# Kernel tuning notes

Hardware: AMD Instinct MI355X
Metric: run time of the kernel (lower is better)

Reference implementation:

```python
import jax, jax.numpy as jnp
import numpy as np

B = 256      # events
N_SV = 64    # secondary vertices per event
N_TRK = 512  # tracks per event
N_PFC = 512  # PF candidates per event
K = 8        # kNN neighbors
H = 32       # hidden dim


def _lin_init(key, fan_in, fan_out):
    k1, k2 = jax.random.split(key)
    lim = 1.0 / np.sqrt(fan_in)
    W = jax.random.uniform(k1, (fan_in, fan_out), minval=-lim, maxval=lim, dtype=jnp.float32)
    b = jax.random.uniform(k2, (fan_out,), minval=-lim, maxval=lim, dtype=jnp.float32)
    return W, b


def setup_inputs() -> dict:
    key = jax.random.key(0)
    ks = jax.random.split(key, 16)
    inp = {
        'x_sv': jax.random.normal(ks[0], (B * N_SV, 14), dtype=jnp.float32),
        'x_trk': jax.random.normal(ks[1], (B * N_TRK, 30), dtype=jnp.float32),
        'x_pfc': jax.random.normal(ks[2], (B * N_PFC, 10), dtype=jnp.float32),
        'batch_sv': jnp.repeat(jnp.arange(B, dtype=jnp.int64), N_SV),
        'batch_trk': jnp.repeat(jnp.arange(B, dtype=jnp.int64), N_TRK),
        'batch_pfc': jnp.repeat(jnp.arange(B, dtype=jnp.int64), N_PFC),
    }
    inp['sv_W1'], inp['sv_b1'] = _lin_init(ks[3], 14, H)
    inp['sv_W2'], inp['sv_b2'] = _lin_init(ks[4], H, H)
    inp['trk_W1'], inp['trk_b1'] = _lin_init(ks[5], 30, H)
    inp['trk_W2'], inp['trk_b2'] = _lin_init(ks[6], H, H)
    inp['pfc_W1'], inp['pfc_b1'] = _lin_init(ks[7], 10, H)
    inp['pfc_W2'], inp['pfc_b2'] = _lin_init(ks[8], H, H)
    inp['conv_W'], inp['conv_b'] = _lin_init(ks[9], 2 * H, H)  # the single shared self.conv
    inp['out_W1'], inp['out_b1'] = _lin_init(ks[10], H, H)
    inp['out_W2'], inp['out_b2'] = _lin_init(ks[11], H, 1)
    return inp


def _encode(x, W1, b1, W2, b2):
    h = jax.nn.elu(x @ W1 + b1)
    return jax.nn.elu(h @ W2 + b2)


def _edge_conv(x_src, x_dst, W, b):
    # x_src [B,Ns,H] source set, x_dst [B,Nd,H] destination/query set.
    # kNN: for each dst node, K nearest src nodes (per event) by Euclidean dist.
    d2 = (jnp.sum(x_dst * x_dst, -1)[:, :, None]
          - 2.0 * jnp.einsum('bnd,bmd->bnm', x_dst, x_src)
          + jnp.sum(x_src * x_src, -1)[:, None, :])  # [B,Nd,Ns]
    _, idx = jax.lax.top_k(-d2, K)                     # [B,Nd,K]
    x_j = jax.vmap(lambda s, i: s[i])(x_src, idx)      # [B,Nd,K,H]
    x_i = jnp.broadcast_to(x_dst[:, :, None, :], x_j.shape)
    e = jnp.concatenate([x_i, x_j - x_i], axis=-1)     # [B,Nd,K,2H]
    m = jax.nn.elu(e @ W + b)                          # edge MLP
    return jnp.max(m, axis=2)                          # max aggregation [B,Nd,H]


def reference(x_sv, x_trk, x_pfc, batch_sv, batch_trk, batch_pfc,
              sv_W1, sv_b1, sv_W2, sv_b2,
              trk_W1, trk_b1, trk_W2, trk_b2,
              pfc_W1, pfc_b1, pfc_W2, pfc_b2,
              conv_W, conv_b, out_W1, out_b1, out_W2, out_b2):
    sv = _encode(x_sv, sv_W1, sv_b1, sv_W2, sv_b2).reshape(B, N_SV, H)
    trk = _encode(x_trk, trk_W1, trk_b1, trk_W2, trk_b2).reshape(B, N_TRK, H)
    pfc = _encode(x_pfc, pfc_W1, pfc_b1, pfc_W2, pfc_b2).reshape(B, N_PFC, H)

    feats1 = _edge_conv(sv, trk, conv_W, conv_b)     # sv -> trk
    feats2 = _edge_conv(pfc, trk, conv_W, conv_b)    # pfc -> trk
    feats3 = _edge_conv(feats1, feats2, conv_W, conv_b)  # feats1 -> feats2 (both trk-sized)

    # avg_pool_x(batch_trk, feats3, batch_trk): per-event mean
    f = feats3.reshape(B * N_TRK, H)
    s = jax.ops.segment_sum(f, batch_trk, num_segments=B)
    cnt = jax.ops.segment_sum(jnp.ones((B * N_TRK,), f.dtype), batch_trk, num_segments=B)
    pooled = s / cnt[:, None]

    out = jax.nn.sigmoid(jax.nn.elu(pooled @ out_W1 + out_b1) @ out_W2 + out_b2)  # [B,1]
    return out, jnp.arange(B, dtype=jnp.int64)
```

## Files before the change

kernel.cpp:

```cpp
#include <hip/hip_runtime.h>
#include <math.h>

#define NB 256
#define KNN 8

typedef __attribute__((ext_vector_type(8))) short short8;
typedef __attribute__((ext_vector_type(4))) float f32x4;

__device__ __forceinline__ float elu_f(float x) {
    return x > 0.f ? x : __expf(x) - 1.f;
}

__device__ __forceinline__ unsigned bf16rn(float x) {
    unsigned u = __float_as_uint(x);
    return (u + 0x7FFFu + ((u >> 16) & 1u)) >> 16;
}

__device__ __forceinline__ void bfsplit(float x, short& h, short& l) {
    unsigned hu = bf16rn(x);
    h = (short)hu;
    l = (short)bf16rn(x - __uint_as_float(hu << 16));
}

__device__ __forceinline__ void cex(unsigned& a, unsigned& b) {
    unsigned lo = min(a, b), hi = max(a, b);
    a = lo; b = hi;
}

__device__ __forceinline__ void sort8(unsigned* s) {
    cex(s[0], s[1]); cex(s[2], s[3]); cex(s[4], s[5]); cex(s[6], s[7]);
    cex(s[0], s[2]); cex(s[1], s[3]); cex(s[4], s[6]); cex(s[5], s[7]);
    cex(s[1], s[2]); cex(s[5], s[6]);
    cex(s[0], s[4]); cex(s[1], s[5]); cex(s[2], s[6]); cex(s[3], s[7]);
    cex(s[2], s[4]); cex(s[3], s[5]);
    cex(s[1], s[2]); cex(s[3], s[4]); cex(s[5], s[6]);
}

__device__ __forceinline__ void merge8(unsigned* v, const unsigned* s) {
#pragma unroll
    for (int i = 0; i < 8; i++) v[i] = min(v[i], s[7 - i]);
    cex(v[0], v[4]); cex(v[1], v[5]); cex(v[2], v[6]); cex(v[3], v[7]);
    cex(v[0], v[2]); cex(v[1], v[3]); cex(v[4], v[6]); cex(v[5], v[7]);
    cex(v[0], v[1]); cex(v[2], v[3]); cex(v[4], v[5]); cex(v[6], v[7]);
}

template<int FIN, int MODE>
__device__ void encode_mfma_body(const float* __restrict__ x,
    const float* __restrict__ W1, const float* __restrict__ b1,
    const float* __restrict__ W2, const float* __restrict__ b2,
    const float* __restrict__ conv_W, const float* __restrict__ conv_b,
    float* __restrict__ enc, float* __restrict__ e1, float* __restrict__ e2,
    unsigned short* __restrict__ hiP, unsigned short* __restrict__ loP,
    float* __restrict__ nrmP,
    int blk, float* __restrict__ sx)
{
    int tid = threadIdx.x;
    int lane = tid & 63, wv = tid >> 6;
    int c = lane & 15, kg = lane >> 4;
    size_t node0 = (size_t)blk * 256;

    {
        const float* xb = x + node0 * FIN;
        for (int i = tid; i < 8192; i += 256) {
            int n = i >> 5, f = i & 31;
            sx[i] = (f < FIN) ? xb[n * FIN + f] : 0.f;
        }
    }
    __syncthreads();

    int rb = wv * 64;

#pragma unroll
    for (int ph = 0; ph < 3; ph++) {
        short8 Bh0, Bl0, Bh1, Bl1;
#pragma unroll
        for (int e = 0; e < 8; e++) {
            int kk = kg * 8 + e;
            float w0, w1;
            if (ph == 0) {
                w0 = (kk < FIN) ? W1[kk * 32 + c] : 0.f;
                w1 = (kk < FIN) ? W1[kk * 32 + 16 + c] : 0.f;
            } else if (ph == 1) {
                w0 = W2[kk * 32 + c];
                w1 = W2[kk * 32 + 16 + c];
            } else {
                w0 = conv_W[1024 + kk * 32 + c];
                w1 = conv_W[1024 + kk * 32 + 16 + c];
                if (MODE == 1) {
                    w0 = conv_W[kk * 32 + c] - w0;
                    w1 = conv_W[kk * 32 + 16 + c] - w1;
                }
            }
            short h, l;
            bfsplit(w0, h, l); Bh0[e] = h; Bl0[e] = l;
            bfsplit(w1, h, l); Bh1[e] = h; Bl1[e] = l;
        }
        float bias0, bias1;
        if (ph == 0)      { bias0 = b1[c]; bias1 = b1[16 + c]; }
        else if (ph == 1) { bias0 = b2[c]; bias1 = b2[16 + c]; }
        else              { bias0 = (MODE == 1) ? conv_b[c] : 0.f;
                            bias1 = (MODE == 1) ? conv_b[16 + c] : 0.f; }

#pragma unroll
        for (int t = 0; t < 4; t++) {
            int tb = rb + t * 16;
            int arow = tb + c;
            const float* ap = sx + arow * 32 + kg * 8;
            float4 a0 = *(const float4*)(ap);
            float4 a1 = *(const float4*)(ap + 4);
            float av[8] = {a0.x, a0.y, a0.z, a0.w, a1.x, a1.y, a1.z, a1.w};
            short8 Ah, Al;
#pragma unroll
            for (int e = 0; e < 8; e++) {
                short h, l;
                bfsplit(av[e], h, l);
                Ah[e] = h; Al[e] = l;
            }

            if (MODE == 0 && ph == 2) {
                float nr = 0.f;
#pragma unroll
                for (int e = 0; e < 8; e++) nr = fmaf(av[e], av[e], nr);
                nr += __shfl_xor(nr, 16);
                nr += __shfl_xor(nr, 32);
                if (kg == 0) nrmP[node0 + arow] = nr;
                *(short8*)(hiP + (node0 + arow) * 32 + kg * 8) = Ah;
                *(short8*)(loP + (node0 + arow) * 32 + kg * 8) = Al;
            }

            f32x4 acc0 = {bias0, bias0, bias0, bias0};
            f32x4 acc1 = {bias1, bias1, bias1, bias1};
            acc0 = __builtin_amdgcn_mfma_f32_16x16x32_bf16(Al, Bh0, acc0, 0, 0, 0);
            acc0 = __builtin_amdgcn_mfma_f32_16x16x32_bf16(Ah, Bl0, acc0, 0, 0, 0);
            acc0 = __builtin_amdgcn_mfma_f32_16x16x32_bf16(Ah, Bh0, acc0, 0, 0, 0);
            acc1 = __builtin_amdgcn_mfma_f32_16x16x32_bf16(Al, Bh1, acc1, 0, 0, 0);
            acc1 = __builtin_amdgcn_mfma_f32_16x16x32_bf16(Ah, Bl1, acc1, 0, 0, 0);
            acc1 = __builtin_amdgcn_mfma_f32_16x16x32_bf16(Ah, Bh1, acc1, 0, 0, 0);

            int drow = tb + kg * 4;
            if (ph < 2) {
#pragma unroll
                for (int r = 0; r < 4; r++) {
                    float v0 = elu_f(acc0[r]);
                    float v1 = elu_f(acc1[r]);
                    sx[(drow + r) * 32 + c] = v0;
                    sx[(drow + r) * 32 + 16 + c] = v1;
                    if (MODE == 1 && ph == 1) {
                        size_t off = (node0 + drow + r) * 32 + c;
                        enc[off] = v0;
                        enc[off + 16] = v1;
                    }
                }
            } else {
#pragma unroll
                for (int r = 0; r < 4; r++) {
                    size_t off = (node0 + drow + r) * 32 + c;
                    e1[off] = acc0[r];
                    e1[off + 16] = acc1[r];
                    if (MODE == 1) {
                        e2[off] = acc0[r];
                        e2[off + 16] = acc1[r];
                    }
                }
            }
        }
    }
}

__global__ __launch_bounds__(256) void encode_all_kernel(
    const float* __restrict__ x_sv, const float* __restrict__ x_trk, const float* __restrict__ x_pfc,
    const float* __restrict__ sv_W1, const float* __restrict__ sv_b1,
    const float* __restrict__ sv_W2, const float* __restrict__ sv_b2,
    const float* __restrict__ trk_W1, const float* __restrict__ trk_b1,
    const float* __restrict__ trk_W2, const float* __restrict__ trk_b2,
    const float* __restrict__ pfc_W1, const float* __restrict__ pfc_b1,
    const float* __restrict__ pfc_W2, const float* __restrict__ pfc_b2,
    const float* __restrict__ conv_W, const float* __restrict__ conv_b,
    float* __restrict__ trk_enc,
    float* __restrict__ Y1, float* __restrict__ Y2,
    float* __restrict__ f1, float* __restrict__ f2,
    unsigned short* __restrict__ svHi, unsigned short* __restrict__ svLo, float* __restrict__ nrm_sv,
    unsigned short* __restrict__ pfcHi, unsigned short* __restrict__ pfcLo, float* __restrict__ nrm_pfc)
{
    __shared__ float sx[8192];
    int bid = blockIdx.x;
    if (bid < 64)
        encode_mfma_body<14, 0>(x_sv, sv_W1, sv_b1, sv_W2, sv_b2, conv_W, conv_b,
                                nullptr, Y1, nullptr, svHi, svLo, nrm_sv, bid, sx);
    else if (bid < 576)
        encode_mfma_body<30, 1>(x_trk, trk_W1, trk_b1, trk_W2, trk_b2, conv_W, conv_b,
                                trk_enc, f1, f2, nullptr, nullptr, nullptr, bid - 64, sx);
    else
        encode_mfma_body<10, 0>(x_pfc, pfc_W1, pfc_b1, pfc_W2, pfc_b2, conv_W, conv_b,
                                nullptr, Y2, nullptr, pfcHi, pfcLo, nrm_pfc, bid - 576, sx);
}

__device__ __forceinline__ void knn_build_B(const float* __restrict__ dstF,
                                            int dstbase, int c, int kg,
                                            short8& Bh, short8& Bl, float& nd)
{
    const float* brow = dstF + (size_t)(dstbase + c) * 32 + kg * 8;
    float4 b0 = *(const float4*)(brow);
    float4 b1 = *(const float4*)(brow + 4);
    float bx[8] = {b0.x, b0.y, b0.z, b0.w, b1.x, b1.y, b1.z, b1.w};
    nd = 0.f;
#pragma unroll
    for (int i = 0; i < 8; i++) {
        float xv = bx[i];
        nd = fmaf(xv, xv, nd);
        short h, l;
        bfsplit(xv, h, l);
        Bh[i] = h; Bl[i] = l;
    }
    nd += __shfl_xor(nd, 16);
    nd += __shfl_xor(nd, 32);
}

template<int NT>
__device__ __forceinline__ void knn_scan(
    const unsigned short* __restrict__ srcHi, const unsigned short* __restrict__ srcLo,
    const float* __restrict__ snrm,
    short8 Bh, short8 Bl, float nd, int c, int kg,
    unsigned* key)
{
    for (int t = 0; t < NT; t += 2) {
        unsigned cand[8];
#pragma unroll
        for (int u = 0; u < 2; u++) {
            int tt = t + u;
            size_t arow = ((size_t)(tt * 16 + c)) * 32 + (size_t)kg * 8;
            short8 Ah = *(const short8*)(srcHi + arow);
            short8 Al = *(const short8*)(srcLo + arow);
            f32x4 acc = {0.f, 0.f, 0.f, 0.f};
            acc = __builtin_amdgcn_mfma_f32_16x16x32_bf16(Al, Bl, acc, 0, 0, 0);
            acc = __builtin_amdgcn_mfma_f32_16x16x32_bf16(Al, Bh, acc, 0, 0, 0);
            acc = __builtin_amdgcn_mfma_f32_16x16x32_bf16(Ah, Bl, acc, 0, 0, 0);
            acc = __builtin_amdgcn_mfma_f32_16x16x32_bf16(Ah, Bh, acc, 0, 0, 0);
            float4 sn = *(const float4*)(snrm + tt * 16 + kg * 4);
            int sb = tt * 16 + kg * 4;
            cand[u*4+0] = (__float_as_uint(fmaf(-2.f, acc[0], sn.x + nd)) & 0xFFFFFE00u) | (unsigned)(sb + 0);
            cand[u*4+1] = (__float_as_uint(fmaf(-2.f, acc[1], sn.y + nd)) & 0xFFFFFE00u) | (unsigned)(sb + 1);
            cand[u*4+2] = (__float_as_uint(fmaf(-2.f, acc[2], sn.z + nd)) & 0xFFFFFE00u) | (unsigned)(sb + 2);
            cand[u*4+3] = (__float_as_uint(fmaf(-2.f, acc[3], sn.w + nd)) & 0xFFFFFE00u) | (unsigned)(sb + 3);
        }
        sort8(cand);
        merge8(key, cand);
    }
}

__device__ __forceinline__ void knn_finalize(unsigned* key, int lane,
                                             unsigned short* __restrict__ idx_out,
                                             int dstbase)
{
    unsigned oth[8];
#pragma unroll
    for (int k = 0; k < 8; k++) oth[k] = __shfl_xor(key[k], 16);
    merge8(key, oth);
#pragma unroll
    for (int k = 0; k < 8; k++) oth[k] = __shfl_xor(key[k], 32);
    merge8(key, oth);
    if (lane < 16) {
        uint4 o;
        o.x = (key[0] & 511u) | ((key[1] & 511u) << 16);
        o.y = (key[2] & 511u) | ((key[3] & 511u) << 16);
        o.z = (key[4] & 511u) | ((key[5] & 511u) << 16);
        o.w = (key[6] & 511u) | ((key[7] & 511u) << 16);
        *(uint4*)(idx_out + (size_t)(dstbase + lane) * 8) = o;
    }
}

__global__ __launch_bounds__(256) void knn12_kernel(
    const unsigned short* __restrict__ svHi, const unsigned short* __restrict__ svLo,
    const float* __restrict__ nrm_sv,
    const unsigned short* __restrict__ pfcHi, const unsigned short* __restrict__ pfcLo,
    const float* __restrict__ nrm_pfc,
    const float* __restrict__ trk_enc,
    unsigned short* __restrict__ idx1, unsigned short* __restrict__ idx2)
{
    int bid = blockIdx.x;
    int e = bid & 255, j = bid >> 8;
    int lane = threadIdx.x & 63, wave = threadIdx.x >> 6;
    int c = lane & 15, kg = lane >> 4;
    int dstbase = j * 64 + wave * 16;

    short8 Bh, Bl;
    float nd;
    knn_build_B(trk_enc + (size_t)e * 512 * 32, dstbase, c, kg, Bh, Bl, nd);

    unsigned key[8];
#pragma unroll
    for (int k = 0; k < 8; k++) key[k] = 0xFFFFFFFFu;
    knn_scan<32>(pfcHi + (size_t)e * 512 * 32, pfcLo + (size_t)e * 512 * 32,
                 nrm_pfc + e * 512, Bh, Bl, nd, c, kg, key);
    knn_finalize(key, lane, idx2 + (size_t)e * 512 * 8, dstbase);

#pragma unroll
    for (int k = 0; k < 8; k++) key[k] = 0xFFFFFFFFu;
    knn_scan<4>(svHi + (size_t)e * 64 * 32, svLo + (size_t)e * 64 * 32,
                nrm_sv + e * 64, Bh, Bl, nd, c, kg, key);
    knn_finalize(key, lane, idx1 + (size_t)e * 512 * 8, dstbase);
}

__global__ __launch_bounds__(256) void knn3_kernel(
    const unsigned short* __restrict__ f1Hi, const unsigned short* __restrict__ f1Lo,
    const float* __restrict__ nrm_f1,
    const float* __restrict__ f2,
    unsigned short* __restrict__ idx3)
{
    int bid = blockIdx.x;
    int e = bid & 255, j = bid >> 8;
    int lane = threadIdx.x & 63, wave = threadIdx.x >> 6;
    int c = lane & 15, kg = lane >> 4;
    int dstbase = j * 64 + wave * 16;

    short8 Bh, Bl;
    float nd;
    knn_build_B(f2 + (size_t)e * 512 * 32, dstbase, c, kg, Bh, Bl, nd);

    unsigned key[8];
#pragma unroll
    for (int k = 0; k < 8; k++) key[k] = 0xFFFFFFFFu;
    knn_scan<32>(f1Hi + (size_t)e * 512 * 32, f1Lo + (size_t)e * 512 * 32,
                 nrm_f1 + e * 512, Bh, Bl, nd, c, kg, key);
    knn_finalize(key, lane, idx3 + (size_t)e * 512 * 8, dstbase);
}

__device__ __forceinline__ void maxgather(const float* __restrict__ Ybase,
                                          const int* rows, float4* m)
{
    const float4* Yb = (const float4*)Ybase;
    const float4* r0 = Yb + (size_t)rows[0] * 8;
#pragma unroll
    for (int q = 0; q < 8; q++) m[q] = r0[q];
#pragma unroll
    for (int k = 1; k < 8; k++) {
        const float4* rr = Yb + (size_t)rows[k] * 8;
#pragma unroll
        for (int q = 0; q < 8; q++) {
            float4 v = rr[q];
            m[q].x = fmaxf(m[q].x, v.x); m[q].y = fmaxf(m[q].y, v.y);
            m[q].z = fmaxf(m[q].z, v.z); m[q].w = fmaxf(m[q].w, v.w);
        }
    }
}

__device__ __forceinline__ void decode_rows(const unsigned short* __restrict__ ip,
                                            size_t t, int* rows)
{
    uint4 u = *(const uint4*)(ip + t * 8);
    rows[0] = (int)(u.x & 0xffff); rows[1] = (int)(u.x >> 16);
    rows[2] = (int)(u.y & 0xffff); rows[3] = (int)(u.y >> 16);
    rows[4] = (int)(u.z & 0xffff); rows[5] = (int)(u.z >> 16);
    rows[6] = (int)(u.w & 0xffff); rows[7] = (int)(u.w >> 16);
}

__global__ __launch_bounds__(256) void g12_kernel(
    const float* __restrict__ Y1, const unsigned short* __restrict__ idx1, float* __restrict__ f1,
    const float* __restrict__ Y2, const unsigned short* __restrict__ idx2, float* __restrict__ f2,
    unsigned short* __restrict__ f1Hi, unsigned short* __restrict__ f1Lo,
    float* __restrict__ nrm_f1)
{
    int bid = blockIdx.x;
    int tid = threadIdx.x;
    int rows[8];
    float* fp;
    const float* Yb;
    int t;
    int isf1 = (bid < 512);
    if (isf1) {
        t = bid * 256 + tid;
        decode_rows(idx1, (size_t)t, rows);
        Yb = Y1 + (size_t)(t >> 9) * 64 * 32;
        fp = f1 + (size_t)t * 32;
    } else {
        t = (bid - 512) * 256 + tid;
        decode_rows(idx2, (size_t)t, rows);
        Yb = Y2 + (size_t)(t >> 9) * 512 * 32;
        fp = f2 + (size_t)t * 32;
    }
    float4 m[8];
    maxgather(Yb, rows, m);
    float4* op = (float4*)fp;
    float4 r[8];
#pragma unroll
    for (int q = 0; q < 8; q++) {
        float4 bv = op[q];
        r[q].x = elu_f(bv.x + m[q].x); r[q].y = elu_f(bv.y + m[q].y);
        r[q].z = elu_f(bv.z + m[q].z); r[q].w = elu_f(bv.w + m[q].w);
        op[q] = r[q];
    }
    if (isf1) {
        unsigned hw[16], lw[16];
        float nr = 0.f;
#pragma unroll
        for (int q = 0; q < 8; q++) {
            float4 v = r[q];
            nr = fmaf(v.x, v.x, nr); nr = fmaf(v.y, v.y, nr);
            nr = fmaf(v.z, v.z, nr); nr = fmaf(v.w, v.w, nr);
            unsigned h0 = bf16rn(v.x), h1 = bf16rn(v.y), h2 = bf16rn(v.z), h3 = bf16rn(v.w);
            unsigned l0 = bf16rn(v.x - __uint_as_float(h0 << 16));
            unsigned l1 = bf16rn(v.y - __uint_as_float(h1 << 16));
            unsigned l2 = bf16rn(v.z - __uint_as_float(h2 << 16));
            unsigned l3 = bf16rn(v.w - __uint_as_float(h3 << 16));
            hw[2*q]   = h0 | (h1 << 16); hw[2*q+1] = h2 | (h3 << 16);
            lw[2*q]   = l0 | (l1 << 16); lw[2*q+1] = l2 | (l3 << 16);
        }
        nrm_f1[t] = nr;
        uint4* hp = (uint4*)(f1Hi + (size_t)t * 32);
        uint4* lp = (uint4*)(f1Lo + (size_t)t * 32);
#pragma unroll
        for (int q = 0; q < 4; q++) {
            hp[q] = make_uint4(hw[4*q], hw[4*q+1], hw[4*q+2], hw[4*q+3]);
            lp[q] = make_uint4(lw[4*q], lw[4*q+1], lw[4*q+2], lw[4*q+3]);
        }
    }
}

__global__ __launch_bounds__(256) void yb3_kernel(
    const float* __restrict__ f1, const float* __restrict__ f2,
    const float* __restrict__ conv_W, const float* __restrict__ conv_b,
    float* __restrict__ Y3, float* __restrict__ B3)
{
    int bid = blockIdx.x;
    int mode = (bid >= 512);
    const float* X = mode ? f2 : f1;
    float* O = mode ? B3 : Y3;
    size_t node0 = (size_t)(mode ? bid - 512 : bid) * 256;
    int tid = threadIdx.x, lane = tid & 63, wv = tid >> 6;
    int c = lane & 15, kg = lane >> 4;

    short8 Bh0, Bl0, Bh1, Bl1;
#pragma unroll
    for (int e = 0; e < 8; e++) {
        int kk = kg * 8 + e;
        float w0 = conv_W[1024 + kk * 32 + c];
        float w1 = conv_W[1024 + kk * 32 + 16 + c];
        if (mode) {
            w0 = conv_W[kk * 32 + c] - w0;
            w1 = conv_W[kk * 32 + 16 + c] - w1;
        }
        short h, l;
        bfsplit(w0, h, l); Bh0[e] = h; Bl0[e] = l;
        bfsplit(w1, h, l); Bh1[e] = h; Bl1[e] = l;
    }
    float bias0 = mode ? conv_b[c] : 0.f;
    float bias1 = mode ? conv_b[16 + c] : 0.f;

    int rb = wv * 64;
#pragma unroll
    for (int t = 0; t < 4; t++) {
        int tb = rb + t * 16;
        int arow = tb + c;
        const float* ap = X + (node0 + arow) * 32 + kg * 8;
        float4 a0 = *(const float4*)(ap);
        float4 a1 = *(const float4*)(ap + 4);
        float av[8] = {a0.x, a0.y, a0.z, a0.w, a1.x, a1.y, a1.z, a1.w};
        short8 Ah, Al;
#pragma unroll
        for (int e = 0; e < 8; e++) {
            short h, l;
            bfsplit(av[e], h, l);
            Ah[e] = h; Al[e] = l;
        }
        f32x4 acc0 = {bias0, bias0, bias0, bias0};
        f32x4 acc1 = {bias1, bias1, bias1, bias1};
        acc0 = __builtin_amdgcn_mfma_f32_16x16x32_bf16(Al, Bh0, acc0, 0, 0, 0);
        acc0 = __builtin_amdgcn_mfma_f32_16x16x32_bf16(Ah, Bl0, acc0, 0, 0, 0);
        acc0 = __builtin_amdgcn_mfma_f32_16x16x32_bf16(Ah, Bh0, acc0, 0, 0, 0);
        acc1 = __builtin_amdgcn_mfma_f32_16x16x32_bf16(Al, Bh1, acc1, 0, 0, 0);
        acc1 = __builtin_amdgcn_mfma_f32_16x16x32_bf16(Ah, Bl1, acc1, 0, 0, 0);
        acc1 = __builtin_amdgcn_mfma_f32_16x16x32_bf16(Ah, Bh1, acc1, 0, 0, 0);

        int drow = tb + kg * 4;
#pragma unroll
        for (int r = 0; r < 4; r++) {
            size_t off = (node0 + drow + r) * 32 + c;
            O[off] = acc0[r];
            O[off + 16] = acc1[r];
        }
    }
}

__global__ __launch_bounds__(256) void g3_kernel(
    const float* __restrict__ Y3, const float* __restrict__ B3,
    const unsigned short* __restrict__ idx3,
    float* __restrict__ pool)
{
    __shared__ float sp[4][32];
    int bid = blockIdx.x;
    int tid = threadIdx.x, lane = tid & 63, wave = tid >> 6;
    int t = bid * 256 + tid;
    int e = t >> 9;
    int rows[8];
    decode_rows(idx3, (size_t)t, rows);
    float4 m[8];
    maxgather(Y3 + (size_t)e * 512 * 32, rows, m);
    const float4* bp = (const float4*)(B3 + (size_t)t * 32);
    float4 r[8];
#pragma unroll
    for (int q = 0; q < 8; q++) {
        float4 bv = bp[q];
        r[q].x = elu_f(bv.x + m[q].x); r[q].y = elu_f(bv.y + m[q].y);
        r[q].z = elu_f(bv.z + m[q].z); r[q].w = elu_f(bv.w + m[q].w);
    }
    for (int off = 1; off < 64; off <<= 1) {
#pragma unroll
        for (int q = 0; q < 8; q++) {
            r[q].x += __shfl_xor(r[q].x, off);
            r[q].y += __shfl_xor(r[q].y, off);
            r[q].z += __shfl_xor(r[q].z, off);
            r[q].w += __shfl_xor(r[q].w, off);
        }
    }
    if (lane == 0) {
#pragma unroll
        for (int q = 0; q < 8; q++) {
            sp[wave][q*4+0] = r[q].x; sp[wave][q*4+1] = r[q].y;
            sp[wave][q*4+2] = r[q].z; sp[wave][q*4+3] = r[q].w;
        }
    }
    __syncthreads();
    if (tid < 32)
        pool[(size_t)bid * 32 + tid] = sp[0][tid] + sp[1][tid] + sp[2][tid] + sp[3][tid];
}

__global__ __launch_bounds__(64) void final_kernel(
    const float* __restrict__ pool,
    const float* __restrict__ W1, const float* __restrict__ b1,
    const float* __restrict__ W2, const float* __restrict__ b2,
    float* __restrict__ outp)
{
    int b = blockIdx.x;
    int lane = threadIdx.x, c = lane & 31;
    __shared__ float sp[32];
    __shared__ float sh1[32];
    if (lane < 32)
        sp[c] = (pool[(size_t)(2*b) * 32 + c] + pool[(size_t)(2*b+1) * 32 + c]) * (1.0f / 512.0f);
    __syncthreads();
    if (lane < 32) {
        float h = b1[c];
#pragma unroll
        for (int d = 0; d < 32; d++) h = fmaf(sp[d], W1[d * 32 + c], h);
        sh1[c] = elu_f(h);
    }
    __syncthreads();
    if (lane == 0) {
        float o = b2[0];
#pragma unroll
        for (int d = 0; d < 32; d++) o = fmaf(sh1[d], W2[d], o);
        o = 1.f / (1.f + __expf(-o));
        outp[b] = o;
        outp[NB + b] = (float)b;
    }
}

extern "C" void kernel_launch(void* const* d_in, const int* in_sizes, int n_in,
                              void* d_out, int out_size, void* d_ws, size_t ws_size,
                              hipStream_t stream) {
    const float* x_sv  = (const float*)d_in[0];
    const float* x_trk = (const float*)d_in[1];
    const float* x_pfc = (const float*)d_in[2];
    const float* sv_W1  = (const float*)d_in[6];
    const float* sv_b1  = (const float*)d_in[7];
    const float* sv_W2  = (const float*)d_in[8];
    const float* sv_b2  = (const float*)d_in[9];
    const float* trk_W1 = (const float*)d_in[10];
    const float* trk_b1 = (const float*)d_in[11];
    const float* trk_W2 = (const float*)d_in[12];
    const float* trk_b2 = (const float*)d_in[13];
    const float* pfc_W1 = (const float*)d_in[14];
    const float* pfc_b1 = (const float*)d_in[15];
    const float* pfc_W2 = (const float*)d_in[16];
    const float* pfc_b2 = (const float*)d_in[17];
    const float* conv_W = (const float*)d_in[18];
    const float* conv_b = (const float*)d_in[19];
    const float* out_W1 = (const float*)d_in[20];
    const float* out_b1 = (const float*)d_in[21];
    const float* out_W2 = (const float*)d_in[22];
    const float* out_b2 = (const float*)d_in[23];

    float* ws = (float*)d_ws;
    const size_t SV_E  = (size_t)NB * 64 * 32;
    const size_t TRK_E = (size_t)NB * 512 * 32;
    float* f1      = ws;
    float* f2      = f1 + TRK_E;
    float* trk_enc = f2 + TRK_E;
    float* Y1      = trk_enc + TRK_E;
    float* Y2      = Y1 + SV_E;
    unsigned short* svHi  = (unsigned short*)(Y2 + TRK_E);
    unsigned short* svLo  = svHi + SV_E;
    unsigned short* pfcHi = svLo + SV_E;
    unsigned short* pfcLo = pfcHi + TRK_E;
    unsigned short* f1Hi  = pfcLo + TRK_E;
    unsigned short* f1Lo  = f1Hi + TRK_E;
    float* nrm_sv  = (float*)(f1Lo + TRK_E);
    float* nrm_pfc = nrm_sv + (size_t)NB * 64;
    float* nrm_f1  = nrm_pfc + (size_t)NB * 512;
    unsigned short* idx1 = (unsigned short*)(nrm_f1 + (size_t)NB * 512);
    unsigned short* idx2 = idx1 + (size_t)NB * 512 * 8;
    unsigned short* idx3 = idx2 + (size_t)NB * 512 * 8;
    float* Y3   = trk_enc;
    float* B3   = (float*)pfcHi;
    float* pool = (float*)svHi;

    encode_all_kernel<<<1088, 256, 0, stream>>>(
        x_sv, x_trk, x_pfc,
        sv_W1, sv_b1, sv_W2, sv_b2,
        trk_W1, trk_b1, trk_W2, trk_b2,
        pfc_W1, pfc_b1, pfc_W2, pfc_b2,
        conv_W, conv_b,
        trk_enc, Y1, Y2, f1, f2,
        svHi, svLo, nrm_sv, pfcHi, pfcLo, nrm_pfc);

    knn12_kernel<<<2048, 256, 0, stream>>>(svHi, svLo, nrm_sv,
                                           pfcHi, pfcLo, nrm_pfc,
                                           trk_enc, idx1, idx2);
    g12_kernel<<<1024, 256, 0, stream>>>(Y1, idx1, f1, Y2, idx2, f2,
                                         f1Hi, f1Lo, nrm_f1);

    yb3_kernel<<<1024, 256, 0, stream>>>(f1, f2, conv_W, conv_b, Y3, B3);
    knn3_kernel<<<2048, 256, 0, stream>>>(f1Hi, f1Lo, nrm_f1, f2, idx3);
    g3_kernel<<<512, 256, 0, stream>>>(Y3, B3, idx3, pool);

    final_kernel<<<NB, 64, 0, stream>>>(pool, out_W1, out_b1, out_W2, out_b2, (float*)d_out);
}
```

Baseline: 316.3 us.

## Fuse kNN gather-max aggregation into kNN kernels, drop index buffers

The separate gather/max kernels (g12, g3) are folded into the kNN kernels. After the lanes merge their top-8 keys, each lane gathers its 8-float slice of the neighbor rows, applies the max, bias and ELU, and writes features, the bf16 hi/lo splits and norms directly. Pooling becomes a per-block partial sum that final_kernel adds across 8 blocks. This removes two launches, the idx1/2/3 round trips and the duplicate f2 write in the encoder. In exchange, gather latency moves into the kNN kernels and adds register pressure there.

After: 303.9 us. -3.9%, faster.

```diff
diff --git a/kernel.cpp b/kernel.cpp
--- a/kernel.cpp
+++ b/kernel.cpp
@@ -49,7 +49,7 @@
     const float* __restrict__ W1, const float* __restrict__ b1,
     const float* __restrict__ W2, const float* __restrict__ b2,
     const float* __restrict__ conv_W, const float* __restrict__ conv_b,
-    float* __restrict__ enc, float* __restrict__ e1, float* __restrict__ e2,
+    float* __restrict__ enc, float* __restrict__ e1,
     unsigned short* __restrict__ hiP, unsigned short* __restrict__ loP,
     float* __restrict__ nrmP,
     int blk, float* __restrict__ sx)
@@ -157,10 +157,6 @@
                     size_t off = (node0 + drow + r) * 32 + c;
                     e1[off] = acc0[r];
                     e1[off + 16] = acc1[r];
-                    if (MODE == 1) {
-                        e2[off] = acc0[r];
-                        e2[off + 16] = acc1[r];
-                    }
                 }
             }
         }
@@ -178,7 +174,7 @@
     const float* __restrict__ conv_W, const float* __restrict__ conv_b,
     float* __restrict__ trk_enc,
     float* __restrict__ Y1, float* __restrict__ Y2,
-    float* __restrict__ f1, float* __restrict__ f2,
+    float* __restrict__ f1,
     unsigned short* __restrict__ svHi, unsigned short* __restrict__ svLo, float* __restrict__ nrm_sv,
     unsigned short* __restrict__ pfcHi, unsigned short* __restrict__ pfcLo, float* __restrict__ nrm_pfc)
 {
@@ -186,13 +182,13 @@
     int bid = blockIdx.x;
     if (bid < 64)
         encode_mfma_body<14, 0>(x_sv, sv_W1, sv_b1, sv_W2, sv_b2, conv_W, conv_b,
-                                nullptr, Y1, nullptr, svHi, svLo, nrm_sv, bid, sx);
+                                nullptr, Y1, svHi, svLo, nrm_sv, bid, sx);
     else if (bid < 576)
         encode_mfma_body<30, 1>(x_trk, trk_W1, trk_b1, trk_W2, trk_b2, conv_W, conv_b,
-                                trk_enc, f1, f2, nullptr, nullptr, nullptr, bid - 64, sx);
+                                trk_enc, f1, nullptr, nullptr, nullptr, bid - 64, sx);
     else
         encode_mfma_body<10, 0>(x_pfc, pfc_W1, pfc_b1, pfc_W2, pfc_b2, conv_W, conv_b,
-                                nullptr, Y2, nullptr, pfcHi, pfcLo, nrm_pfc, bid - 576, sx);
+                                nullptr, Y2, pfcHi, pfcLo, nrm_pfc, bid - 576, sx);
 }
 
 __device__ __forceinline__ void knn_build_B(const float* __restrict__ dstF,
@@ -248,9 +244,7 @@
     }
 }
 
-__device__ __forceinline__ void knn_finalize(unsigned* key, int lane,
-                                             unsigned short* __restrict__ idx_out,
-                                             int dstbase)
+__device__ __forceinline__ void knn_merge_lanes(unsigned* key)
 {
     unsigned oth[8];
 #pragma unroll
@@ -259,13 +253,25 @@
 #pragma unroll
     for (int k = 0; k < 8; k++) oth[k] = __shfl_xor(key[k], 32);
     merge8(key, oth);
-    if (lane < 16) {
-        uint4 o;
-        o.x = (key[0] & 511u) | ((key[1] & 511u) << 16);
-        o.y = (key[2] & 511u) | ((key[3] & 511u) << 16);
-        o.z = (key[4] & 511u) | ((key[5] & 511u) << 16);
-        o.w = (key[6] & 511u) | ((key[7] & 511u) << 16);
-        *(uint4*)(idx_out + (size_t)(dstbase + lane) * 8) = o;
+}
+
+__device__ __forceinline__ void gather_max8(const float* __restrict__ Yb,
+                                            const unsigned* key, int kg, float* m)
+{
+    const float* r0 = Yb + (size_t)(key[0] & 511u) * 32 + kg * 8;
+    float4 a = *(const float4*)(r0);
+    float4 b = *(const float4*)(r0 + 4);
+    m[0] = a.x; m[1] = a.y; m[2] = a.z; m[3] = a.w;
+    m[4] = b.x; m[5] = b.y; m[6] = b.z; m[7] = b.w;
+#pragma unroll
+    for (int k = 1; k < 8; k++) {
+        const float* rr = Yb + (size_t)(key[k] & 511u) * 32 + kg * 8;
+        float4 va = *(const float4*)(rr);
+        float4 vb = *(const float4*)(rr + 4);
+        m[0] = fmaxf(m[0], va.x); m[1] = fmaxf(m[1], va.y);
+        m[2] = fmaxf(m[2], va.z); m[3] = fmaxf(m[3], va.w);
+        m[4] = fmaxf(m[4], vb.x); m[5] = fmaxf(m[5], vb.y);
+        m[6] = fmaxf(m[6], vb.z); m[7] = fmaxf(m[7], vb.w);
     }
 }
 
@@ -275,43 +281,91 @@
     const unsigned short* __restrict__ pfcHi, const unsigned short* __restrict__ pfcLo,
     const float* __restrict__ nrm_pfc,
     const float* __restrict__ trk_enc,
-    unsigned short* __restrict__ idx1, unsigned short* __restrict__ idx2)
+    const float* __restrict__ Y1, const float* __restrict__ Y2,
+    float* __restrict__ f1, float* __restrict__ f2,
+    unsigned short* __restrict__ f1Hi, unsigned short* __restrict__ f1Lo,
+    float* __restrict__ nrm_f1)
 {
     int bid = blockIdx.x;
     int e = bid & 255, j = bid >> 8;
     int lane = threadIdx.x & 63, wave = threadIdx.x >> 6;
     int c = lane & 15, kg = lane >> 4;
     int dstbase = j * 64 + wave * 16;
+    size_t trow = (size_t)e * 512 + dstbase + c;
 
     short8 Bh, Bl;
     float nd;
     knn_build_B(trk_enc + (size_t)e * 512 * 32, dstbase, c, kg, Bh, Bl, nd);
 
-    unsigned key[8];
-#pragma unroll
-    for (int k = 0; k < 8; k++) key[k] = 0xFFFFFFFFu;
+    unsigned key2[8];
+#pragma unroll
+    for (int k = 0; k < 8; k++) key2[k] = 0xFFFFFFFFu;
     knn_scan<32>(pfcHi + (size_t)e * 512 * 32, pfcLo + (size_t)e * 512 * 32,
-                 nrm_pfc + e * 512, Bh, Bl, nd, c, kg, key);
-    knn_finalize(key, lane, idx2 + (size_t)e * 512 * 8, dstbase);
-
-#pragma unroll
-    for (int k = 0; k < 8; k++) key[k] = 0xFFFFFFFFu;
+                 nrm_pfc + e * 512, Bh, Bl, nd, c, kg, key2);
+    knn_merge_lanes(key2);
+
+    unsigned key1[8];
+#pragma unroll
+    for (int k = 0; k < 8; k++) key1[k] = 0xFFFFFFFFu;
     knn_scan<4>(svHi + (size_t)e * 64 * 32, svLo + (size_t)e * 64 * 32,
-                nrm_sv + e * 64, Bh, Bl, nd, c, kg, key);
-    knn_finalize(key, lane, idx1 + (size_t)e * 512 * 8, dstbase);
+                nrm_sv + e * 64, Bh, Bl, nd, c, kg, key1);
+    knn_merge_lanes(key1);
+
+    const float* bp = f1 + trow * 32 + kg * 8;
+    float4 bb0 = *(const float4*)(bp);
+    float4 bb1 = *(const float4*)(bp + 4);
+    float base[8] = {bb0.x, bb0.y, bb0.z, bb0.w, bb1.x, bb1.y, bb1.z, bb1.w};
+
+    float m[8];
+    gather_max8(Y2 + (size_t)e * 512 * 32, key2, kg, m);
+    {
+        float4 o0, o1;
+        o0.x = elu_f(base[0] + m[0]); o0.y = elu_f(base[1] + m[1]);
+        o0.z = elu_f(base[2] + m[2]); o0.w = elu_f(base[3] + m[3]);
+        o1.x = elu_f(base[4] + m[4]); o1.y = elu_f(base[5] + m[5]);
+        o1.z = elu_f(base[6] + m[6]); o1.w = elu_f(base[7] + m[7]);
+        float4* op = (float4*)(f2 + trow * 32 + kg * 8);
+        op[0] = o0; op[1] = o1;
+    }
+    gather_max8(Y1 + (size_t)e * 64 * 32, key1, kg, m);
+    {
+        float v[8];
+        float nr = 0.f;
+        short8 Hh, Hl;
+#pragma unroll
+        for (int i = 0; i < 8; i++) {
+            v[i] = elu_f(base[i] + m[i]);
+            nr = fmaf(v[i], v[i], nr);
+            short h, l;
+            bfsplit(v[i], h, l);
+            Hh[i] = h; Hl[i] = l;
+        }
+        nr += __shfl_xor(nr, 16);
+        nr += __shfl_xor(nr, 32);
+        if (kg == 0) nrm_f1[trow] = nr;
+        float4* op = (float4*)(f1 + trow * 32 + kg * 8);
+        op[0] = (float4){v[0], v[1], v[2], v[3]};
+        op[1] = (float4){v[4], v[5], v[6], v[7]};
+        *(short8*)(f1Hi + trow * 32 + kg * 8) = Hh;
+        *(short8*)(f1Lo + trow * 32 + kg * 8) = Hl;
+    }
 }
 
 __global__ __launch_bounds__(256) void knn3_kernel(
     const unsigned short* __restrict__ f1Hi, const unsigned short* __restrict__ f1Lo,
     const float* __restrict__ nrm_f1,
     const float* __restrict__ f2,
-    unsigned short* __restrict__ idx3)
-{
+    const float* __restrict__ Y3, const float* __restrict__ B3,
+    float* __restrict__ pool)
+{
+    __shared__ float sp[4][32];
     int bid = blockIdx.x;
     int e = bid & 255, j = bid >> 8;
-    int lane = threadIdx.x & 63, wave = threadIdx.x >> 6;
+    int tid = threadIdx.x;
+    int lane = tid & 63, wave = tid >> 6;
     int c = lane & 15, kg = lane >> 4;
     int dstbase = j * 64 + wave * 16;
+    size_t trow = (size_t)e * 512 + dstbase + c;
 
     short8 Bh, Bl;
     float nd;
@@ -322,98 +376,33 @@
     for (int k = 0; k < 8; k++) key[k] = 0xFFFFFFFFu;
     knn_scan<32>(f1Hi + (size_t)e * 512 * 32, f1Lo + (size_t)e * 512 * 32,
                  nrm_f1 + e * 512, Bh, Bl, nd, c, kg, key);
-    knn_finalize(key, lane, idx3 + (size_t)e * 512 * 8, dstbase);
-}
-
-__device__ __forceinline__ void maxgather(const float* __restrict__ Ybase,
-                                          const int* rows, float4* m)
-{
-    const float4* Yb = (const float4*)Ybase;
-    const float4* r0 = Yb + (size_t)rows[0] * 8;
-#pragma unroll
-    for (int q = 0; q < 8; q++) m[q] = r0[q];
-#pragma unroll
-    for (int k = 1; k < 8; k++) {
-        const float4* rr = Yb + (size_t)rows[k] * 8;
-#pragma unroll
-        for (int q = 0; q < 8; q++) {
-            float4 v = rr[q];
-            m[q].x = fmaxf(m[q].x, v.x); m[q].y = fmaxf(m[q].y, v.y);
-            m[q].z = fmaxf(m[q].z, v.z); m[q].w = fmaxf(m[q].w, v.w);
-        }
-    }
-}
-
-__device__ __forceinline__ void decode_rows(const unsigned short* __restrict__ ip,
-                                            size_t t, int* rows)
-{
-    uint4 u = *(const uint4*)(ip + t * 8);
-    rows[0] = (int)(u.x & 0xffff); rows[1] = (int)(u.x >> 16);
-    rows[2] = (int)(u.y & 0xffff); rows[3] = (int)(u.y >> 16);
-    rows[4] = (int)(u.z & 0xffff); rows[5] = (int)(u.z >> 16);
-    rows[6] = (int)(u.w & 0xffff); rows[7] = (int)(u.w >> 16);
-}
-
-__global__ __launch_bounds__(256) void g12_kernel(
-    const float* __restrict__ Y1, const unsigned short* __restrict__ idx1, float* __restrict__ f1,
-    const float* __restrict__ Y2, const unsigned short* __restrict__ idx2, float* __restrict__ f2,
-    unsigned short* __restrict__ f1Hi, unsigned short* __restrict__ f1Lo,
-    float* __restrict__ nrm_f1)
-{
-    int bid = blockIdx.x;
-    int tid = threadIdx.x;
-    int rows[8];
-    float* fp;
-    const float* Yb;
-    int t;
-    int isf1 = (bid < 512);
-    if (isf1) {
-        t = bid * 256 + tid;
-        decode_rows(idx1, (size_t)t, rows);
-        Yb = Y1 + (size_t)(t >> 9) * 64 * 32;
-        fp = f1 + (size_t)t * 32;
-    } else {
-        t = (bid - 512) * 256 + tid;
-        decode_rows(idx2, (size_t)t, rows);
-        Yb = Y2 + (size_t)(t >> 9) * 512 * 32;
-        fp = f2 + (size_t)t * 32;
-    }
-    float4 m[8];
-    maxgather(Yb, rows, m);
-    float4* op = (float4*)fp;
-    float4 r[8];
-#pragma unroll
-    for (int q = 0; q < 8; q++) {
-        float4 bv = op[q];
-        r[q].x = elu_f(bv.x + m[q].x); r[q].y = elu_f(bv.y + m[q].y);
-        r[q].z = elu_f(bv.z + m[q].z); r[q].w = elu_f(bv.w + m[q].w);
-        op[q] = r[q];
-    }
-    if (isf1) {
-        unsigned hw[16], lw[16];
-        float nr = 0.f;
-#pragma unroll
-        for (int q = 0; q < 8; q++) {
-            float4 v = r[q];
-            nr = fmaf(v.x, v.x, nr); nr = fmaf(v.y, v.y, nr);
-            nr = fmaf(v.z, v.z, nr); nr = fmaf(v.w, v.w, nr);
-            unsigned h0 = bf16rn(v.x), h1 = bf16rn(v.y), h2 = bf16rn(v.z), h3 = bf16rn(v.w);
-            unsigned l0 = bf16rn(v.x - __uint_as_float(h0 << 16));
-            unsigned l1 = bf16rn(v.y - __uint_as_float(h1 << 16));
-            unsigned l2 = bf16rn(v.z - __uint_as_float(h2 << 16));
-            unsigned l3 = bf16rn(v.w - __uint_as_float(h3 << 16));
-            hw[2*q]   = h0 | (h1 << 16); hw[2*q+1] = h2 | (h3 << 16);
-            lw[2*q]   = l0 | (l1 << 16); lw[2*q+1] = l2 | (l3 << 16);
-        }
-        nrm_f1[t] = nr;
-        uint4* hp = (uint4*)(f1Hi + (size_t)t * 32);
-        uint4* lp = (uint4*)(f1Lo + (size_t)t * 32);
-#pragma unroll
-        for (int q = 0; q < 4; q++) {
-            hp[q] = make_uint4(hw[4*q], hw[4*q+1], hw[4*q+2], hw[4*q+3]);
-            lp[q] = make_uint4(lw[4*q], lw[4*q+1], lw[4*q+2], lw[4*q+3]);
-        }
-    }
+    knn_merge_lanes(key);
+
+    float m[8];
+    gather_max8(Y3 + (size_t)e * 512 * 32, key, kg, m);
+
+    const float* bp = B3 + trow * 32 + kg * 8;
+    float4 bb0 = *(const float4*)(bp);
+    float4 bb1 = *(const float4*)(bp + 4);
+    float base[8] = {bb0.x, bb0.y, bb0.z, bb0.w, bb1.x, bb1.y, bb1.z, bb1.w};
+
+    float r[8];
+#pragma unroll
+    for (int i = 0; i < 8; i++) r[i] = elu_f(base[i] + m[i]);
+
+#pragma unroll
+    for (int off = 1; off < 16; off <<= 1) {
+#pragma unroll
+        for (int i = 0; i < 8; i++) r[i] += __shfl_xor(r[i], off);
+    }
+    if (c == 0) {
+#pragma unroll
+        for (int i = 0; i < 8; i++) sp[wave][kg * 8 + i] = r[i];
+    }
+    __syncthreads();
+    if (tid < 32)
+        pool[((size_t)e * 8 + j) * 32 + tid] =
+            sp[0][tid] + sp[1][tid] + sp[2][tid] + sp[3][tid];
 }
 
 __global__ __launch_bounds__(256) void yb3_kernel(
@@ -481,49 +470,6 @@
     }
 }
 
-__global__ __launch_bounds__(256) void g3_kernel(
-    const float* __restrict__ Y3, const float* __restrict__ B3,
-    const unsigned short* __restrict__ idx3,
-    float* __restrict__ pool)
-{
-    __shared__ float sp[4][32];
-    int bid = blockIdx.x;
-    int tid = threadIdx.x, lane = tid & 63, wave = tid >> 6;
-    int t = bid * 256 + tid;
-    int e = t >> 9;
-    int rows[8];
-    decode_rows(idx3, (size_t)t, rows);
-    float4 m[8];
-    maxgather(Y3 + (size_t)e * 512 * 32, rows, m);
-    const float4* bp = (const float4*)(B3 + (size_t)t * 32);
-    float4 r[8];
-#pragma unroll
-    for (int q = 0; q < 8; q++) {
-        float4 bv = bp[q];
-        r[q].x = elu_f(bv.x + m[q].x); r[q].y = elu_f(bv.y + m[q].y);
-        r[q].z = elu_f(bv.z + m[q].z); r[q].w = elu_f(bv.w + m[q].w);
-    }
-    for (int off = 1; off < 64; off <<= 1) {
-#pragma unroll
-        for (int q = 0; q < 8; q++) {
-            r[q].x += __shfl_xor(r[q].x, off);
-            r[q].y += __shfl_xor(r[q].y, off);
-            r[q].z += __shfl_xor(r[q].z, off);
-            r[q].w += __shfl_xor(r[q].w, off);
-        }
-    }
-    if (lane == 0) {
-#pragma unroll
-        for (int q = 0; q < 8; q++) {
-            sp[wave][q*4+0] = r[q].x; sp[wave][q*4+1] = r[q].y;
-            sp[wave][q*4+2] = r[q].z; sp[wave][q*4+3] = r[q].w;
-        }
-    }
-    __syncthreads();
-    if (tid < 32)
-        pool[(size_t)bid * 32 + tid] = sp[0][tid] + sp[1][tid] + sp[2][tid] + sp[3][tid];
-}
-
 __global__ __launch_bounds__(64) void final_kernel(
     const float* __restrict__ pool,
     const float* __restrict__ W1, const float* __restrict__ b1,
@@ -534,8 +480,13 @@
     int lane = threadIdx.x, c = lane & 31;
     __shared__ float sp[32];
     __shared__ float sh1[32];
-    if (lane < 32)
-        sp[c] = (pool[(size_t)(2*b) * 32 + c] + pool[(size_t)(2*b+1) * 32 + c]) * (1.0f / 512.0f);
+    if (lane < 32) {
+        float s = 0.f;
+#pragma unroll
+        for (int jj = 0; jj < 8; jj++)
+            s += pool[((size_t)b * 8 + jj) * 32 + c];
+        sp[c] = s * (1.0f / 512.0f);
+    }
     __syncthreads();
     if (lane < 32) {
         float h = b1[c];
@@ -596,9 +547,6 @@
     float* nrm_sv  = (float*)(f1Lo + TRK_E);
     float* nrm_pfc = nrm_sv + (size_t)NB * 64;
     float* nrm_f1  = nrm_pfc + (size_t)NB * 512;
-    unsigned short* idx1 = (unsigned short*)(nrm_f1 + (size_t)NB * 512);
-    unsigned short* idx2 = idx1 + (size_t)NB * 512 * 8;
-    unsigned short* idx3 = idx2 + (size_t)NB * 512 * 8;
     float* Y3   = trk_enc;
     float* B3   = (float*)pfcHi;
     float* pool = (float*)svHi;
@@ -609,18 +557,16 @@
         trk_W1, trk_b1, trk_W2, trk_b2,
         pfc_W1, pfc_b1, pfc_W2, pfc_b2,
         conv_W, conv_b,
-        trk_enc, Y1, Y2, f1, f2,
+        trk_enc, Y1, Y2, f1,
         svHi, svLo, nrm_sv, pfcHi, pfcLo, nrm_pfc);
 
     knn12_kernel<<<2048, 256, 0, stream>>>(svHi, svLo, nrm_sv,
                                            pfcHi, pfcLo, nrm_pfc,
-                                           trk_enc, idx1, idx2);
-    g12_kernel<<<1024, 256, 0, stream>>>(Y1, idx1, f1, Y2, idx2, f2,
-                                         f1Hi, f1Lo, nrm_f1);
+                                           trk_enc, Y1, Y2,
+                                           f1, f2, f1Hi, f1Lo, nrm_f1);
 
     yb3_kernel<<<1024, 256, 0, stream>>>(f1, f2, conv_W, conv_b, Y3, B3);
-    knn3_kernel<<<2048, 256, 0, stream>>>(f1Hi, f1Lo, nrm_f1, f2, idx3);
-    g3_kernel<<<512, 256, 0, stream>>>(Y3, B3, idx3, pool);
+    knn3_kernel<<<2048, 256, 0, stream>>>(f1Hi, f1Lo, nrm_f1, f2, Y3, B3, pool);
 
     final_kernel<<<NB, 64, 0, stream>>>(pool, out_W1, out_b1, out_W2, out_b2, (float*)d_out);
 }
```
